# Performance work log

Hardware: AMD Instinct MI355X
Metric: run time of the kernel (lower is better)

The kernel has to match this reference:

```python
import jax, jax.numpy as jnp
import numpy as np

B, S, E, H = 2, 2048, 1280, 20
D = E // H  # head_dim = 64
SCALING = D ** -0.5


def setup_inputs() -> dict:
    key = jax.random.key(0)
    k1, k2, k3, k4, k5 = jax.random.split(key, 5)
    return {
        "hidden_states": jax.random.normal(k1, (B, S, E), dtype=jnp.float32),
        "qkv_w": jax.random.normal(k2, (E, 3 * E), dtype=jnp.float32) * (E ** -0.5),
        "qkv_b": jax.random.normal(k3, (3 * E,), dtype=jnp.float32) * 0.02,
        "out_w": jax.random.normal(k4, (E, E), dtype=jnp.float32) * (E ** -0.5),
        "out_b": jax.random.normal(k5, (E,), dtype=jnp.float32) * 0.02,
    }


def reference(hidden_states, qkv_w, qkv_b, out_w, out_b):
    b, s, e = hidden_states.shape
    # fused QKV projection
    qkv = hidden_states @ qkv_w + qkv_b              # [B,S,3E]
    q, k, v = jnp.split(qkv, 3, axis=-1)
    q = q * SCALING                                  # module pre-scales q; attn uses scaling=1.0
    q = q.reshape(b, s, H, D)
    k = k.reshape(b, s, H, D)
    v = v.reshape(b, s, H, D)
    scores = jnp.einsum("bqhd,bkhd->bhqk", q, k)     # [B,H,S,S]
    # decoder (causal) attention, per AttentionType.DECODER
    causal = jnp.tril(jnp.ones((s, s), dtype=bool))
    scores = jnp.where(causal[None, None], scores, jnp.finfo(scores.dtype).min)
    probs = jax.nn.softmax(scores, axis=-1)
    attn = jnp.einsum("bhqk,bkhd->bqhd", probs, v).reshape(b, s, e)
    return attn @ out_w + out_b
```

## Files before the change

### kernel.cpp

```cpp
#include <hip/hip_runtime.h>
#include <stdint.h>

typedef unsigned short u16;
typedef short s8v __attribute__((ext_vector_type(8)));
typedef float f32x4 __attribute__((ext_vector_type(4)));

#define NB 2
#define NH 20
#define SEQ 2048
#define EMB 1280
#define HD 64
#define MT (NB*SEQ)
#define N3E (3*EMB)
#define QSCALE 0.18033688011112042f

__device__ __forceinline__ u16 f2bf(float f){
  unsigned u = __float_as_uint(f);
  u += 0x7fffu + ((u >> 16) & 1u);
  return (u16)(u >> 16);
}

__global__ __launch_bounds__(256) void prep_kernel(
    const float* __restrict__ hs, const float* __restrict__ qkv_w,
    const float* __restrict__ out_w,
    u16* __restrict__ xb, u16* __restrict__ wqkvT, u16* __restrict__ woT)
{
  __shared__ float tl[32][33];
  int blk = blockIdx.x;
  if (blk < 5120){
    int i = blk*256 + threadIdx.x;
    float4 f = ((const float4* __restrict__)hs)[i];
    ushort4 o;
    o.x = f2bf(f.x); o.y = f2bf(f.y); o.z = f2bf(f.z); o.w = f2bf(f.w);
    ((ushort4*)xb)[i] = o;
    return;
  }
  const float* in; u16* out; int R, C, bx, by;
  if (blk < 9920){
    int b2 = blk - 5120; bx = b2 % 120; by = b2 / 120;
    in = qkv_w; out = wqkvT; R = EMB; C = N3E;
  } else {
    int b2 = blk - 9920; bx = b2 % 40; by = b2 / 40;
    in = out_w; out = woT; R = EMB; C = EMB;
  }
  int c0 = bx*32, r0 = by*32;
  int tx = threadIdx.x & 31, ty = threadIdx.x >> 5;
  #pragma unroll
  for (int i=0;i<4;i++)
    tl[ty + i*8][tx] = in[(size_t)(r0 + ty + i*8)*C + c0 + tx];
  __syncthreads();
  #pragma unroll
  for (int i=0;i<4;i++)
    out[(size_t)(c0 + ty + i*8)*R + r0 + tx] = f2bf(tl[tx][ty + i*8]);
}

template<int NIT>
__device__ __forceinline__ void stage_swz(const u16* gsrc, int ld, u16* lds, int t){
  #pragma unroll
  for (int i=0;i<NIT;i++){
    int f = i*256 + t;
    int row = f >> 3, sl = f & 7;
    int ssl = sl ^ (row & 7);
    __builtin_amdgcn_global_load_lds(
      (const __attribute__((address_space(1))) void*)(gsrc + (size_t)row*ld + ssl*8),
      (__attribute__((address_space(3))) void*)(lds + f*8), 16, 0, 0);
  }
}

__device__ __forceinline__ s8v frag_ld(const u16* lds, int row, int ks){
  int sl = ks ^ (row & 7);
  return *(const s8v*)(lds + row*64 + sl*8);
}

template<int EPI>
__global__ __launch_bounds__(256) void gemm_bt_kernel(
    const u16* __restrict__ A, const u16* __restrict__ Bt, const float* __restrict__ bias,
    float* __restrict__ Cout, int Ntot, int K,
    u16* __restrict__ qb, u16* __restrict__ kbf, u16* __restrict__ vT)
{
  __shared__ u16 As[128*64];
  __shared__ u16 Bs[128*64];
  int t = threadIdx.x;
  int lane = t & 63, w = t >> 6;
  int wr = w >> 1, wc = w & 1;
  int g = lane >> 4, c = lane & 15;
  int m0 = blockIdx.y*128, n0 = blockIdx.x*128;
  f32x4 acc[4][4] = {};
  for (int k0 = 0; k0 < K; k0 += 64){
    stage_swz<4>(A  + (size_t)m0*K + k0, K, As, t);
    stage_swz<4>(Bt + (size_t)n0*K + k0, K, Bs, t);
    __syncthreads();
    #pragma unroll
    for (int kb2=0;kb2<2;kb2++){
      s8v af[4], bfr[4];
      #pragma unroll
      for (int m=0;m<4;m++) af[m]  = frag_ld(As, wr*64 + m*16 + c, kb2*4 + g);
      #pragma unroll
      for (int n=0;n<4;n++) bfr[n] = frag_ld(Bs, wc*64 + n*16 + c, kb2*4 + g);
      #pragma unroll
      for (int m=0;m<4;m++)
        #pragma unroll
        for (int n=0;n<4;n++)
          acc[m][n] = __builtin_amdgcn_mfma_f32_16x16x32_bf16(af[m], bfr[n], acc[m][n], 0, 0, 0);
    }
    __syncthreads();
  }
  #pragma unroll
  for (int m=0;m<4;m++){
    int growb = m0 + wr*64 + m*16 + g*4;
    #pragma unroll
    for (int n=0;n<4;n++){
      int gcol = n0 + wc*64 + n*16 + c;
      float bv = bias[gcol];
      if (EPI == 1){
        #pragma unroll
        for (int r=0;r<4;r++)
          Cout[(size_t)(growb + r)*Ntot + gcol] = acc[m][n][r] + bv;
      } else {
        int which = gcol / EMB;
        int e = gcol - which*EMB;
        int hh = e >> 6, d = e & 63;
        int bi = growb >> 11, sb = growb & 2047;
        size_t bh = (size_t)bi*NH + hh;
        if (which == 2){
          ushort4 pv;
          pv.x = f2bf(acc[m][n][0] + bv);
          pv.y = f2bf(acc[m][n][1] + bv);
          pv.z = f2bf(acc[m][n][2] + bv);
          pv.w = f2bf(acc[m][n][3] + bv);
          *(ushort4*)(vT + (bh*HD + d)*SEQ + sb) = pv;
        } else {
          u16* dst = (which == 0) ? qb : kbf;
          float scl = (which == 0) ? QSCALE : 1.0f;
          #pragma unroll
          for (int r=0;r<4;r++)
            dst[(bh*SEQ + sb + r)*HD + d] = f2bf((acc[m][n][r] + bv)*scl);
        }
      }
    }
  }
}

__global__ __launch_bounds__(256) void attn_kernel(
    const u16* __restrict__ qb, const u16* __restrict__ kbf, const u16* __restrict__ vT,
    u16* __restrict__ attn)
{
  __shared__ u16 Kls[2][64*64];
  __shared__ u16 Vls[2][64*64];
  __shared__ u16 Ps[4][16*72];
  int bh = blockIdx.x;
  int b = bh / NH, h = bh - b*NH;
  int qt = 31 - blockIdx.y;
  int t = threadIdx.x, lane = t & 63, w = t >> 6;
  int g = lane >> 4, c = lane & 15;
  u16* pw = &Ps[w][0];
  const u16* Kb = kbf + (size_t)bh*SEQ*HD;
  const u16* Vb = vT  + (size_t)bh*HD*SEQ;

  int qwb = qt*64 + w*16;
  const u16* qrow = qb + ((size_t)bh*SEQ + qwb + c)*HD;
  s8v aq0 = *(const s8v*)(qrow + g*8);
  s8v aq1 = *(const s8v*)(qrow + 32 + g*8);
  f32x4 po[4] = {};
  float mrow = -1e30f, lrow = 0.f;

  stage_swz<2>(Kb, HD, Kls[0], t);
  stage_swz<2>(Vb, SEQ, Vls[0], t);

  for (int kt = 0; kt <= qt; ++kt){
    int cur = kt & 1;
    const u16* Ks = Kls[cur];
    const u16* Vs = Vls[cur];
    if (kt < qt){
      int k1 = (kt + 1)*64;
      stage_swz<2>(Kb + (size_t)k1*HD, HD,  Kls[cur^1], t);
      stage_swz<2>(Vb + k1,            SEQ, Vls[cur^1], t);
      asm volatile("s_waitcnt vmcnt(4)" ::: "memory");
    } else {
      asm volatile("s_waitcnt vmcnt(0)" ::: "memory");
    }
    __builtin_amdgcn_s_barrier();
    __builtin_amdgcn_sched_barrier(0);

    int k0 = kt*64;
    s8v vv[8];
    #pragma unroll
    for (int kb2=0;kb2<2;kb2++)
      #pragma unroll
      for (int dt=0;dt<4;dt++)
        vv[kb2*4+dt] = frag_ld(Vs, dt*16 + c, kb2*4 + g);
    f32x4 sc[4];
    __builtin_amdgcn_s_setprio(1);
    #pragma unroll
    for (int nt=0;nt<4;nt++){
      s8v k0f = frag_ld(Ks, nt*16 + c, g);
      s8v k1f = frag_ld(Ks, nt*16 + c, 4 + g);
      f32x4 z = {0.f,0.f,0.f,0.f};
      sc[nt] = __builtin_amdgcn_mfma_f32_16x16x32_bf16(k0f, aq0, z,      0,0,0);
      sc[nt] = __builtin_amdgcn_mfma_f32_16x16x32_bf16(k1f, aq1, sc[nt], 0,0,0);
    }
    __builtin_amdgcn_s_setprio(0);
    if (kt == qt){
      #pragma unroll
      for (int nt=0;nt<4;nt++){
        int kg = k0 + nt*16 + g*4;
        #pragma unroll
        for (int r=0;r<4;r++)
          if (kg + r > qwb + c) sc[nt][r] = -1e30f;
      }
    }
    float mt = fmaxf(fmaxf(sc[0][0],sc[0][1]), fmaxf(sc[0][2],sc[0][3]));
    #pragma unroll
    for (int nt=1;nt<4;nt++)
      mt = fmaxf(mt, fmaxf(fmaxf(sc[nt][0],sc[nt][1]), fmaxf(sc[nt][2],sc[nt][3])));
    mt = fmaxf(mt, __shfl_xor(mt, 16));
    mt = fmaxf(mt, __shfl_xor(mt, 32));
    if (!__all(mt - mrow <= 8.0f)){
      float mn = fmaxf(mrow, mt);
      float alpha = exp2f(mrow - mn);
      mrow = mn;
      lrow *= alpha;
      float alB[4];
      #pragma unroll
      for (int r=0;r<4;r++)
        alB[r] = __shfl(alpha, (lane & 48) | (g*4 + r));
      #pragma unroll
      for (int dt=0;dt<4;dt++)
        #pragma unroll
        for (int r=0;r<4;r++)
          po[dt][r] *= alB[r];
    }
    float rs = 0.f;
    #pragma unroll
    for (int nt=0;nt<4;nt++)
      #pragma unroll
      for (int r=0;r<4;r++){
        float pe = exp2f(sc[nt][r] - mrow);
        sc[nt][r] = pe;
        rs += pe;
      }
    rs += __shfl_xor(rs, 16);
    rs += __shfl_xor(rs, 32);
    lrow += rs;
    #pragma unroll
    for (int nt=0;nt<4;nt++){
      ushort4 pk;
      pk.x = f2bf(sc[nt][0]); pk.y = f2bf(sc[nt][1]);
      pk.z = f2bf(sc[nt][2]); pk.w = f2bf(sc[nt][3]);
      *(ushort4*)(pw + c*72 + nt*16 + g*4) = pk;
    }
    __builtin_amdgcn_s_setprio(1);
    #pragma unroll
    for (int kb2=0;kb2<2;kb2++){
      s8v pa = *(const s8v*)(pw + c*72 + kb2*32 + g*8);
      #pragma unroll
      for (int dt=0;dt<4;dt++)
        po[dt] = __builtin_amdgcn_mfma_f32_16x16x32_bf16(pa, vv[kb2*4+dt], po[dt], 0,0,0);
    }
    __builtin_amdgcn_s_setprio(0);
    asm volatile("s_waitcnt lgkmcnt(0)" ::: "memory");
    __builtin_amdgcn_s_barrier();
  }
  float inv = 1.0f / lrow;
  float invB[4];
  #pragma unroll
  for (int r=0;r<4;r++)
    invB[r] = __shfl(inv, (lane & 48) | (g*4 + r));
  #pragma unroll
  for (int dt=0;dt<4;dt++){
    #pragma unroll
    for (int r=0;r<4;r++){
      int qa = qwb + g*4 + r;
      attn[((size_t)(b*SEQ + qa))*EMB + h*HD + dt*16 + c] = f2bf(po[dt][r] * invB[r]);
    }
  }
}

extern "C" void kernel_launch(void* const* d_in, const int* in_sizes, int n_in,
                              void* d_out, int out_size, void* d_ws, size_t ws_size,
                              hipStream_t stream) {
  const float* hs    = (const float*)d_in[0];
  const float* qkv_w = (const float*)d_in[1];
  const float* qkv_b = (const float*)d_in[2];
  const float* out_w = (const float*)d_in[3];
  const float* out_b = (const float*)d_in[4];
  float* out = (float*)d_out;

  char* p = (char*)d_ws;
  u16* xb    = (u16*)p; p += (size_t)MT*EMB*2;
  u16* wqkvT = (u16*)p; p += (size_t)N3E*EMB*2;
  u16* woT   = (u16*)p; p += (size_t)EMB*EMB*2;
  u16* qbuf  = (u16*)p; p += (size_t)NB*NH*SEQ*HD*2;
  u16* kbuf  = (u16*)p; p += (size_t)NB*NH*SEQ*HD*2;
  u16* vTb   = (u16*)p; p += (size_t)NB*NH*SEQ*HD*2;
  u16* attnb = (u16*)p; p += (size_t)MT*EMB*2;

  prep_kernel<<<11520, 256, 0, stream>>>(hs, qkv_w, out_w, xb, wqkvT, woT);
  gemm_bt_kernel<0><<<dim3(N3E/128, MT/128), 256, 0, stream>>>(
      xb, wqkvT, qkv_b, nullptr, N3E, EMB, qbuf, kbuf, vTb);
  attn_kernel<<<dim3(40, 32), 256, 0, stream>>>(qbuf, kbuf, vTb, attnb);
  gemm_bt_kernel<1><<<dim3(EMB/128, MT/128), 256, 0, stream>>>(
      attnb, woT, out_b, out, EMB, EMB, nullptr, nullptr, nullptr);
}
```

Baseline: 254.3 us.

## Transpose PV MFMA output layout, swizzle P LDS buffer, use packed bf16 converts

```diff
diff --git a/kernel.cpp b/kernel.cpp
--- a/kernel.cpp
+++ b/kernel.cpp
@@ -1,4 +1,5 @@
 #include <hip/hip_runtime.h>
+#include <hip/hip_bf16.h>
 #include <stdint.h>
 
 typedef unsigned short u16;
@@ -18,6 +19,11 @@
   unsigned u = __float_as_uint(f);
   u += 0x7fffu + ((u >> 16) & 1u);
   return (u16)(u >> 16);
+}
+
+__device__ __forceinline__ unsigned pk2(float a, float b){
+  __hip_bfloat162 h = __float22bfloat162_rn(float2{a, b});
+  return *reinterpret_cast<unsigned*>(&h);
 }
 
 __global__ __launch_bounds__(256) void prep_kernel(
@@ -123,12 +129,10 @@
         int bi = growb >> 11, sb = growb & 2047;
         size_t bh = (size_t)bi*NH + hh;
         if (which == 2){
-          ushort4 pv;
-          pv.x = f2bf(acc[m][n][0] + bv);
-          pv.y = f2bf(acc[m][n][1] + bv);
-          pv.z = f2bf(acc[m][n][2] + bv);
-          pv.w = f2bf(acc[m][n][3] + bv);
-          *(ushort4*)(vT + (bh*HD + d)*SEQ + sb) = pv;
+          uint2 pv2;
+          pv2.x = pk2(acc[m][n][0] + bv, acc[m][n][1] + bv);
+          pv2.y = pk2(acc[m][n][2] + bv, acc[m][n][3] + bv);
+          *(uint2*)(vT + (bh*HD + d)*SEQ + sb) = pv2;
         } else {
           u16* dst = (which == 0) ? qb : kbf;
           float scl = (which == 0) ? QSCALE : 1.0f;
@@ -147,7 +151,7 @@
 {
   __shared__ u16 Kls[2][64*64];
   __shared__ u16 Vls[2][64*64];
-  __shared__ u16 Ps[4][16*72];
+  __shared__ u16 Ps[4][1024];
   int bh = blockIdx.x;
   int b = bh / NH, h = bh - b*NH;
   int qt = 31 - blockIdx.y;
@@ -163,6 +167,7 @@
   s8v aq1 = *(const s8v*)(qrow + 32 + g*8);
   f32x4 po[4] = {};
   float mrow = -1e30f, lrow = 0.f;
+  int cswz = 2*(c & 7);
 
   stage_swz<2>(Kb, HD, Kls[0], t);
   stage_swz<2>(Vb, SEQ, Vls[0], t);
@@ -220,15 +225,11 @@
       float alpha = exp2f(mrow - mn);
       mrow = mn;
       lrow *= alpha;
-      float alB[4];
-      #pragma unroll
-      for (int r=0;r<4;r++)
-        alB[r] = __shfl(alpha, (lane & 48) | (g*4 + r));
       #pragma unroll
       for (int dt=0;dt<4;dt++)
         #pragma unroll
         for (int r=0;r<4;r++)
-          po[dt][r] *= alB[r];
+          po[dt][r] *= alpha;
     }
     float rs = 0.f;
     #pragma unroll
@@ -244,35 +245,31 @@
     lrow += rs;
     #pragma unroll
     for (int nt=0;nt<4;nt++){
-      ushort4 pk;
-      pk.x = f2bf(sc[nt][0]); pk.y = f2bf(sc[nt][1]);
-      pk.z = f2bf(sc[nt][2]); pk.w = f2bf(sc[nt][3]);
-      *(ushort4*)(pw + c*72 + nt*16 + g*4) = pk;
+      uint2 pk;
+      pk.x = pk2(sc[nt][0], sc[nt][1]);
+      pk.y = pk2(sc[nt][2], sc[nt][3]);
+      *(uint2*)(pw + c*64 + ((nt*4 + g) ^ cswz)*4) = pk;
     }
     __builtin_amdgcn_s_setprio(1);
     #pragma unroll
     for (int kb2=0;kb2<2;kb2++){
-      s8v pa = *(const s8v*)(pw + c*72 + kb2*32 + g*8);
+      s8v pa = *(const s8v*)(pw + c*64 + ((kb2*8 + 2*g) ^ cswz)*4);
       #pragma unroll
       for (int dt=0;dt<4;dt++)
-        po[dt] = __builtin_amdgcn_mfma_f32_16x16x32_bf16(pa, vv[kb2*4+dt], po[dt], 0,0,0);
+        po[dt] = __builtin_amdgcn_mfma_f32_16x16x32_bf16(vv[kb2*4+dt], pa, po[dt], 0,0,0);
     }
     __builtin_amdgcn_s_setprio(0);
     asm volatile("s_waitcnt lgkmcnt(0)" ::: "memory");
     __builtin_amdgcn_s_barrier();
   }
   float inv = 1.0f / lrow;
-  float invB[4];
-  #pragma unroll
-  for (int r=0;r<4;r++)
-    invB[r] = __shfl(inv, (lane & 48) | (g*4 + r));
+  const size_t orow = ((size_t)(b*SEQ + qwb + c))*EMB + h*HD;
   #pragma unroll
   for (int dt=0;dt<4;dt++){
-    #pragma unroll
-    for (int r=0;r<4;r++){
-      int qa = qwb + g*4 + r;
-      attn[((size_t)(b*SEQ + qa))*EMB + h*HD + dt*16 + c] = f2bf(po[dt][r] * invB[r]);
-    }
+    uint2 o;
+    o.x = pk2(po[dt][0]*inv, po[dt][1]*inv);
+    o.y = pk2(po[dt][2]*inv, po[dt][3]*inv);
+    *(uint2*)(attn + orow + dt*16 + g*4) = o;
   }
 }
 
```

New measurement: 252.2 us. About the same (-0.8%).
